# Performance work log

Hardware: AMD Instinct MI355X
Metric: run time of the kernel (lower is better)

The kernel has to match this reference:

```python
import jax, jax.numpy as jnp
import numpy as np

IN_F = 4096
OUT_F = 4096
RANK = 16
ALPHA = 32.0


def setup_inputs() -> dict:
    key = jax.random.key(0)
    k1, k2, k3, k4, k5 = jax.random.split(key, 5)
    x = jax.random.normal(k1, (4, 2048, IN_F), dtype=jnp.float32)
    W = jax.random.normal(k2, (OUT_F, IN_F), dtype=jnp.float32) * (1.0 / np.sqrt(IN_F))
    b = jax.random.normal(k3, (OUT_F,), dtype=jnp.float32) * 0.01
    # torch init: lora_A ~ uniform(0.01, 1.0) per nn.init.uniform_(a=0.01); lora_B zeros.
    # Use nonzero B here so the adapter path is numerically exercised.
    lora_A = jax.random.uniform(k4, (RANK, IN_F), dtype=jnp.float32, minval=0.01, maxval=1.0)
    lora_B = jax.random.normal(k5, (OUT_F, RANK), dtype=jnp.float32) * 0.01
    return {"x": x, "W": W, "b": b, "lora_A": lora_A, "lora_B": lora_B}


def reference(x, W, b, lora_A, lora_B):
    scaling = ALPHA / RANK
    # base linear: x @ W.T + b   -> [B, S, out]
    base = jnp.einsum("bsi,oi->bso", x, W) + b
    # low-rank adapter: (x @ A.T) @ B.T * scaling
    xa = jnp.einsum("bsi,ri->bsr", x, lora_A)        # [B, S, rank]
    adj = jnp.einsum("bsr,or->bso", xa, lora_B) * scaling
    return base + adj
```

## Files before the change

### kernel.cpp

```cpp
#include <hip/hip_runtime.h>
#include <hip/hip_bf16.h>
#include <stdint.h>

#define MM 8192
#define NN 4096
#define KK 4096
#define RANK 16
#define SCALING 2.0f

typedef __bf16 bf16x8 __attribute__((ext_vector_type(8)));
typedef float  f32x4  __attribute__((ext_vector_type(4)));

__device__ inline void async_copy16(const void* g, void* lds) {
    __builtin_amdgcn_global_load_lds(
        (const __attribute__((address_space(1))) void*)g,
        (__attribute__((address_space(3))) void*)lds,
        16, 0, 0);
}

__global__ void conv_bf16_kernel(const float* __restrict__ src,
                                 __hip_bfloat16* __restrict__ dst, int n8) {
    int i = blockIdx.x * blockDim.x + threadIdx.x;
    if (i >= n8) return;
    const float4* s = (const float4*)src + (size_t)i * 2;
    float4 a = s[0], b = s[1];
    union { __hip_bfloat16 h[8]; uint4 u; } o;
    o.h[0] = __float2bfloat16(a.x); o.h[1] = __float2bfloat16(a.y);
    o.h[2] = __float2bfloat16(a.z); o.h[3] = __float2bfloat16(a.w);
    o.h[4] = __float2bfloat16(b.x); o.h[5] = __float2bfloat16(b.y);
    o.h[6] = __float2bfloat16(b.z); o.h[7] = __float2bfloat16(b.w);
    *((uint4*)dst + (size_t)i) = o.u;
}

__global__ void prep_w_kernel(const float* __restrict__ W,
                              const float* __restrict__ lA,
                              const float* __restrict__ lB,
                              __hip_bfloat16* __restrict__ dst) {
    int idx = blockIdx.x * blockDim.x + threadIdx.x;
    int o  = idx >> 9;
    int i0 = (idx & 511) << 3;
    const float4* wp = (const float4*)(W + (size_t)o * KK + i0);
    float4 w0 = wp[0], w1 = wp[1];
    float acc[8] = {0,0,0,0,0,0,0,0};
#pragma unroll
    for (int r = 0; r < RANK; ++r) {
        float bv = lB[o * RANK + r];
        const float4* ap = (const float4*)(lA + (size_t)r * KK + i0);
        float4 a0 = ap[0], a1 = ap[1];
        acc[0] += bv * a0.x; acc[1] += bv * a0.y;
        acc[2] += bv * a0.z; acc[3] += bv * a0.w;
        acc[4] += bv * a1.x; acc[5] += bv * a1.y;
        acc[6] += bv * a1.z; acc[7] += bv * a1.w;
    }
    float res[8] = { w0.x + SCALING * acc[0], w0.y + SCALING * acc[1],
                     w0.z + SCALING * acc[2], w0.w + SCALING * acc[3],
                     w1.x + SCALING * acc[4], w1.y + SCALING * acc[5],
                     w1.z + SCALING * acc[6], w1.w + SCALING * acc[7] };
    union { __hip_bfloat16 h[8]; uint4 u; } pk;
#pragma unroll
    for (int j = 0; j < 8; ++j) pk.h[j] = __float2bfloat16(res[j]);
    *((uint4*)dst + (size_t)idx) = pk.u;
}

#define BM 128
#define BN 128
#define BK 32

__global__ __launch_bounds__(256, 3)
void gemm_bt_kernel(const __hip_bfloat16* __restrict__ A,
                    const __hip_bfloat16* __restrict__ B,
                    const float* __restrict__ bias,
                    float* __restrict__ C) {
    __shared__ __align__(16) __hip_bfloat16 As[BM * BK];
    __shared__ __align__(16) __hip_bfloat16 Bs[BN * BK];

    const int t    = threadIdx.x;
    const int lane = t & 63;
    const int wave = t >> 6;
    const int wm   = wave >> 1;
    const int wn   = wave & 1;
    const int row16 = lane & 15;
    const int quad  = lane >> 4;
    const int bm = blockIdx.y, bn = blockIdx.x;

    f32x4 acc[4][4] = {};

    const int srow   = t >> 2;
    const int schunk = (t & 3) * 8;
    const __hip_bfloat16* gA0 = A + (size_t)(bm * BM + srow) * KK + schunk;
    const __hip_bfloat16* gA1 = gA0 + (size_t)64 * KK;
    const __hip_bfloat16* gB0 = B + (size_t)(bn * BN + srow) * KK + schunk;
    const __hip_bfloat16* gB1 = gB0 + (size_t)64 * KK;

    char* ldsA = (char*)As + wave * 1024;
    char* ldsB = (char*)Bs + wave * 1024;

    for (int kt = 0; kt < KK; kt += BK) {
        async_copy16(gA0 + kt, ldsA);
        async_copy16(gA1 + kt, ldsA + 4096);
        async_copy16(gB0 + kt, ldsB);
        async_copy16(gB1 + kt, ldsB + 4096);
        __syncthreads();

        bf16x8 af[4], bg[4];
#pragma unroll
        for (int mi = 0; mi < 4; ++mi)
            af[mi] = *(const bf16x8*)(As + (wm * 64 + mi * 16 + row16) * BK + quad * 8);
#pragma unroll
        for (int ni = 0; ni < 4; ++ni)
            bg[ni] = *(const bf16x8*)(Bs + (wn * 64 + ni * 16 + row16) * BK + quad * 8);
#pragma unroll
        for (int mi = 0; mi < 4; ++mi)
#pragma unroll
            for (int ni = 0; ni < 4; ++ni)
                acc[mi][ni] = __builtin_amdgcn_mfma_f32_16x16x32_bf16(
                    af[mi], bg[ni], acc[mi][ni], 0, 0, 0);
        __syncthreads();
    }

    const int colBase = bn * BN + wn * 64;
    const int rowBase = bm * BM + wm * 64;
#pragma unroll
    for (int ni = 0; ni < 4; ++ni) {
        int col = colBase + ni * 16 + row16;
        float bv = bias[col];
#pragma unroll
        for (int mi = 0; mi < 4; ++mi) {
            int r0 = rowBase + mi * 16 + quad * 4;
#pragma unroll
            for (int i = 0; i < 4; ++i)
                C[(size_t)(r0 + i) * NN + col] = acc[mi][ni][i] + bv;
        }
    }
}

__global__ void naive_base_kernel(const float* __restrict__ x,
                                  const float* __restrict__ W,
                                  const float* __restrict__ b,
                                  float* __restrict__ out) {
    size_t idx = (size_t)blockIdx.x * 256 + threadIdx.x;
    int m = (int)(idx / NN), n = (int)(idx % NN);
    const float* xr = x + (size_t)m * KK;
    const float* wr = W + (size_t)n * KK;
    float s = 0.f;
    for (int k = 0; k < KK; ++k) s += xr[k] * wr[k];
    out[idx] = s + b[n];
}

__global__ void naive_adapter_kernel(const float* __restrict__ x,
                                     const float* __restrict__ lA,
                                     const float* __restrict__ lB,
                                     float* __restrict__ out) {
    int m = blockIdx.x;
    __shared__ float xa[RANK];
    __shared__ float red[256];
    const float* xr = x + (size_t)m * KK;
    for (int r = 0; r < RANK; ++r) {
        float p = 0.f;
        for (int k = threadIdx.x; k < KK; k += 256) p += xr[k] * lA[(size_t)r * KK + k];
        red[threadIdx.x] = p;
        __syncthreads();
        for (int s = 128; s > 0; s >>= 1) {
            if (threadIdx.x < s) red[threadIdx.x] += red[threadIdx.x + s];
            __syncthreads();
        }
        if (threadIdx.x == 0) xa[r] = red[0];
        __syncthreads();
    }
    for (int n = threadIdx.x; n < NN; n += 256) {
        float adj = 0.f;
#pragma unroll
        for (int r = 0; r < RANK; ++r) adj += xa[r] * lB[n * RANK + r];
        out[(size_t)m * NN + n] += SCALING * adj;
    }
}

extern "C" void kernel_launch(void* const* d_in, const int* in_sizes, int n_in,
                              void* d_out, int out_size, void* d_ws, size_t ws_size,
                              hipStream_t stream) {
    const float* x  = (const float*)d_in[0];
    const float* W  = (const float*)d_in[1];
    const float* b  = (const float*)d_in[2];
    const float* lA = (const float*)d_in[3];
    const float* lB = (const float*)d_in[4];
    float* out = (float*)d_out;

    size_t need = (size_t)MM * KK * 2 + (size_t)NN * KK * 2;
    if (ws_size >= need) {
        __hip_bfloat16* xb = (__hip_bfloat16*)d_ws;
        __hip_bfloat16* wb = xb + (size_t)MM * KK;
        conv_bf16_kernel<<<(MM * KK / 8 + 255) / 256, 256, 0, stream>>>(x, xb, MM * KK / 8);
        prep_w_kernel<<<(NN * KK / 8 + 255) / 256, 256, 0, stream>>>(W, lA, lB, wb);
        gemm_bt_kernel<<<dim3(NN / BN, MM / BM), 256, 0, stream>>>(xb, wb, b, out);
    } else {
        naive_base_kernel<<<(size_t)MM * NN / 256, 256, 0, stream>>>(x, W, b, out);
        naive_adapter_kernel<<<MM, 256, 0, stream>>>(x, lA, lB, out);
    }
}
```

Before: 630.7 us.

## Merge prep kernels, swizzle LDS, remap blocks per XCD, raise occupancy bound

Merges the x conversion and the W+LoRA folding into one launch so a kernel boundary and launch gap go away. In the GEMM, the LDS chunk index is XOR-swizzled on both the async write side and the fragment read side to cut bank conflicts. A 1D grid is remapped so each XCD gets a contiguous 16x16 tile region, improving L2 reuse of A and B. The launch bound rises from 3 to 4 blocks per CU, which may force register spills.

```diff
diff --git a/kernel.cpp b/kernel.cpp
--- a/kernel.cpp
+++ b/kernel.cpp
@@ -18,55 +18,59 @@
         16, 0, 0);
 }
 
-__global__ void conv_bf16_kernel(const float* __restrict__ src,
-                                 __hip_bfloat16* __restrict__ dst, int n8) {
-    int i = blockIdx.x * blockDim.x + threadIdx.x;
-    if (i >= n8) return;
-    const float4* s = (const float4*)src + (size_t)i * 2;
-    float4 a = s[0], b = s[1];
-    union { __hip_bfloat16 h[8]; uint4 u; } o;
-    o.h[0] = __float2bfloat16(a.x); o.h[1] = __float2bfloat16(a.y);
-    o.h[2] = __float2bfloat16(a.z); o.h[3] = __float2bfloat16(a.w);
-    o.h[4] = __float2bfloat16(b.x); o.h[5] = __float2bfloat16(b.y);
-    o.h[6] = __float2bfloat16(b.z); o.h[7] = __float2bfloat16(b.w);
-    *((uint4*)dst + (size_t)i) = o.u;
-}
-
-__global__ void prep_w_kernel(const float* __restrict__ W,
-                              const float* __restrict__ lA,
-                              const float* __restrict__ lB,
-                              __hip_bfloat16* __restrict__ dst) {
-    int idx = blockIdx.x * blockDim.x + threadIdx.x;
-    int o  = idx >> 9;
-    int i0 = (idx & 511) << 3;
-    const float4* wp = (const float4*)(W + (size_t)o * KK + i0);
-    float4 w0 = wp[0], w1 = wp[1];
-    float acc[8] = {0,0,0,0,0,0,0,0};
-#pragma unroll
-    for (int r = 0; r < RANK; ++r) {
-        float bv = lB[o * RANK + r];
-        const float4* ap = (const float4*)(lA + (size_t)r * KK + i0);
-        float4 a0 = ap[0], a1 = ap[1];
-        acc[0] += bv * a0.x; acc[1] += bv * a0.y;
-        acc[2] += bv * a0.z; acc[3] += bv * a0.w;
-        acc[4] += bv * a1.x; acc[5] += bv * a1.y;
-        acc[6] += bv * a1.z; acc[7] += bv * a1.w;
-    }
-    float res[8] = { w0.x + SCALING * acc[0], w0.y + SCALING * acc[1],
-                     w0.z + SCALING * acc[2], w0.w + SCALING * acc[3],
-                     w1.x + SCALING * acc[4], w1.y + SCALING * acc[5],
-                     w1.z + SCALING * acc[6], w1.w + SCALING * acc[7] };
-    union { __hip_bfloat16 h[8]; uint4 u; } pk;
-#pragma unroll
-    for (int j = 0; j < 8; ++j) pk.h[j] = __float2bfloat16(res[j]);
-    *((uint4*)dst + (size_t)idx) = pk.u;
+#define CONV_BLOCKS 16384
+#define PREP_BLOCKS 8192
+
+__global__ void pre_kernel(const float* __restrict__ x,
+                           const float* __restrict__ W,
+                           const float* __restrict__ lA,
+                           const float* __restrict__ lB,
+                           __hip_bfloat16* __restrict__ xb,
+                           __hip_bfloat16* __restrict__ wb) {
+    int bid = blockIdx.x;
+    if (bid < CONV_BLOCKS) {
+        size_t i = (size_t)bid * 256 + threadIdx.x;
+        const float4* s = (const float4*)x + i * 2;
+        float4 a = s[0], b = s[1];
+        union { __hip_bfloat16 h[8]; uint4 u; } o;
+        o.h[0] = __float2bfloat16(a.x); o.h[1] = __float2bfloat16(a.y);
+        o.h[2] = __float2bfloat16(a.z); o.h[3] = __float2bfloat16(a.w);
+        o.h[4] = __float2bfloat16(b.x); o.h[5] = __float2bfloat16(b.y);
+        o.h[6] = __float2bfloat16(b.z); o.h[7] = __float2bfloat16(b.w);
+        *((uint4*)xb + i) = o.u;
+    } else {
+        size_t idx = (size_t)(bid - CONV_BLOCKS) * 256 + threadIdx.x;
+        int o  = (int)(idx >> 9);
+        int i0 = ((int)idx & 511) << 3;
+        const float4* wp = (const float4*)(W + (size_t)o * KK + i0);
+        float4 w0 = wp[0], w1 = wp[1];
+        float acc[8] = {0,0,0,0,0,0,0,0};
+#pragma unroll
+        for (int r = 0; r < RANK; ++r) {
+            float bv = lB[o * RANK + r];
+            const float4* ap = (const float4*)(lA + (size_t)r * KK + i0);
+            float4 a0 = ap[0], a1 = ap[1];
+            acc[0] += bv * a0.x; acc[1] += bv * a0.y;
+            acc[2] += bv * a0.z; acc[3] += bv * a0.w;
+            acc[4] += bv * a1.x; acc[5] += bv * a1.y;
+            acc[6] += bv * a1.z; acc[7] += bv * a1.w;
+        }
+        float res[8] = { w0.x + SCALING * acc[0], w0.y + SCALING * acc[1],
+                         w0.z + SCALING * acc[2], w0.w + SCALING * acc[3],
+                         w1.x + SCALING * acc[4], w1.y + SCALING * acc[5],
+                         w1.z + SCALING * acc[6], w1.w + SCALING * acc[7] };
+        union { __hip_bfloat16 h[8]; uint4 u; } pk;
+#pragma unroll
+        for (int j = 0; j < 8; ++j) pk.h[j] = __float2bfloat16(res[j]);
+        *((uint4*)wb + idx) = pk.u;
+    }
 }
 
 #define BM 128
 #define BN 128
 #define BK 32
 
-__global__ __launch_bounds__(256, 3)
+__global__ __launch_bounds__(256, 4)
 void gemm_bt_kernel(const __hip_bfloat16* __restrict__ A,
                     const __hip_bfloat16* __restrict__ B,
                     const float* __restrict__ bias,
@@ -74,19 +78,24 @@
     __shared__ __align__(16) __hip_bfloat16 As[BM * BK];
     __shared__ __align__(16) __hip_bfloat16 Bs[BN * BK];
 
-    const int t    = threadIdx.x;
-    const int lane = t & 63;
-    const int wave = t >> 6;
-    const int wm   = wave >> 1;
-    const int wn   = wave & 1;
+    const int t     = threadIdx.x;
+    const int lane  = t & 63;
+    const int wave  = t >> 6;
+    const int wm    = wave >> 1;
+    const int wn    = wave & 1;
     const int row16 = lane & 15;
     const int quad  = lane >> 4;
-    const int bm = blockIdx.y, bn = blockIdx.x;
+
+    const int id  = blockIdx.x;
+    const int xcd = id & 7;
+    const int lid = id >> 3;
+    const int bm  = (xcd >> 1) * 16 + (lid >> 4);
+    const int bn  = (xcd & 1) * 16 + (lid & 15);
 
     f32x4 acc[4][4] = {};
 
     const int srow   = t >> 2;
-    const int schunk = (t & 3) * 8;
+    const int schunk = ((t & 3) ^ ((t >> 3) & 3)) * 8;
     const __hip_bfloat16* gA0 = A + (size_t)(bm * BM + srow) * KK + schunk;
     const __hip_bfloat16* gA1 = gA0 + (size_t)64 * KK;
     const __hip_bfloat16* gB0 = B + (size_t)(bn * BN + srow) * KK + schunk;
@@ -94,6 +103,8 @@
 
     char* ldsA = (char*)As + wave * 1024;
     char* ldsB = (char*)Bs + wave * 1024;
+
+    const int sw = (quad ^ ((row16 >> 1) & 3)) * 8;
 
     for (int kt = 0; kt < KK; kt += BK) {
         async_copy16(gA0 + kt, ldsA);
@@ -105,10 +116,10 @@
         bf16x8 af[4], bg[4];
 #pragma unroll
         for (int mi = 0; mi < 4; ++mi)
-            af[mi] = *(const bf16x8*)(As + (wm * 64 + mi * 16 + row16) * BK + quad * 8);
+            af[mi] = *(const bf16x8*)(As + (wm * 64 + mi * 16 + row16) * BK + sw);
 #pragma unroll
         for (int ni = 0; ni < 4; ++ni)
-            bg[ni] = *(const bf16x8*)(Bs + (wn * 64 + ni * 16 + row16) * BK + quad * 8);
+            bg[ni] = *(const bf16x8*)(Bs + (wn * 64 + ni * 16 + row16) * BK + sw);
 #pragma unroll
         for (int mi = 0; mi < 4; ++mi)
 #pragma unroll
@@ -189,9 +200,8 @@
     if (ws_size >= need) {
         __hip_bfloat16* xb = (__hip_bfloat16*)d_ws;
         __hip_bfloat16* wb = xb + (size_t)MM * KK;
-        conv_bf16_kernel<<<(MM * KK / 8 + 255) / 256, 256, 0, stream>>>(x, xb, MM * KK / 8);
-        prep_w_kernel<<<(NN * KK / 8 + 255) / 256, 256, 0, stream>>>(W, lA, lB, wb);
-        gemm_bt_kernel<<<dim3(NN / BN, MM / BM), 256, 0, stream>>>(xb, wb, b, out);
+        pre_kernel<<<CONV_BLOCKS + PREP_BLOCKS, 256, 0, stream>>>(x, W, lA, lB, xb, wb);
+        gemm_bt_kernel<<<(MM / BM) * (NN / BN), 256, 0, stream>>>(xb, wb, b, out);
     } else {
         naive_base_kernel<<<(size_t)MM * NN / 256, 256, 0, stream>>>(x, W, b, out);
         naive_adapter_kernel<<<MM, 256, 0, stream>>>(x, lA, lB, out);
```

New measurement: 631.3 us. About the same (+0.1%).
